# Kernel optimization log

Measured on AMD Instinct MI355X. Metric: run time of the kernel, lower is better.

## Reference

```python
import jax, jax.numpy as jnp
import numpy as np


def setup_inputs() -> dict:
    key = jax.random.key(0)
    ks = jax.random.split(key, 8)
    B, L, E, U = 32, 2048, 1024, 1024
    s = 0.02
    return {
        "dec_hidden": jax.random.normal(ks[0], (B, E), jnp.float32),
        "enc_output": jax.random.normal(ks[1], (B, L, E), jnp.float32),
        "prev_coverage": jax.random.uniform(ks[2], (B, L, 1), jnp.float32),
        "Ws_k": jax.random.normal(ks[3], (E, U), jnp.float32) * s,
        "Ws_b": jnp.zeros((U,), jnp.float32),
        "Wh_k": jax.random.normal(ks[4], (E, U), jnp.float32) * s,
        "Wh_b": jnp.zeros((U,), jnp.float32),
        "Wc_k": jax.random.normal(ks[5], (1, U), jnp.float32) * s,
        "Wc_b": jnp.zeros((U,), jnp.float32),
        "V_k": jax.random.normal(ks[6], (U, 1), jnp.float32) * s,
        "V_b": jnp.zeros((1,), jnp.float32),
        "enc_pad_mask": jnp.ones((B, L), jnp.int32),
        "use_coverage": 1,
    }


def reference(dec_hidden, enc_output, prev_coverage, Ws_k, Ws_b, Wh_k, Wh_b,
              Wc_k, Wc_b, V_k, V_b, enc_pad_mask, use_coverage):
    # projections: [B,L,U] + [B,1,U] (+ [B,L,U] coverage term)
    pre = jnp.einsum('ble,eu->blu', enc_output, Ws_k) + Ws_b \
        + (dec_hidden @ Wh_k + Wh_b)[:, None, :]
    if use_coverage:
        pre = pre + (prev_coverage @ Wc_k + Wc_b)
    score = jnp.tanh(pre) @ V_k + V_b              # [B, L, 1]
    mask = enc_pad_mask.astype(score.dtype)        # [B, L]
    masked_score = (score[..., 0] * mask)[..., None]  # [B, L, 1]
    attention_weights = jax.nn.softmax(masked_score, axis=1)
    coverage = attention_weights + prev_coverage if use_coverage else attention_weights
    context_vector = jnp.sum(attention_weights * enc_output, axis=1)  # [B, E]
    return (context_vector, attention_weights, coverage)
```

## Files before the change

### kernel.cpp

```cpp
#include <hip/hip_runtime.h>
#include <hip/hip_bf16.h>
#include <math.h>

typedef float f32x4 __attribute__((ext_vector_type(4)));
typedef short short8 __attribute__((ext_vector_type(8)));
typedef unsigned short u16x8 __attribute__((ext_vector_type(8)));

static __device__ __forceinline__ unsigned short f2bf(float f) {
    unsigned u = __builtin_bit_cast(unsigned, f);
    unsigned r = (u + 0x7FFFu + ((u >> 16) & 1u)) >> 16;
    return (unsigned short)r;
}
static __device__ __forceinline__ float bf2f(unsigned short h) {
    unsigned u = ((unsigned)h) << 16;
    return __builtin_bit_cast(float, u);
}
static __device__ __forceinline__ float fast_tanh(float x) {
    float ax = fminf(fmaxf(x, -9.f), 9.f);
    float e = __expf(2.f * ax);
    return 1.f - 2.f / (e + 1.f);
}

#define GLD16(g, l) __builtin_amdgcn_global_load_lds(                        \
    (const __attribute__((address_space(1))) void*)(g),                      \
    (__attribute__((address_space(3))) void*)(l), 16, 0, 0)

__global__ __launch_bounds__(256) void prep_kernel(
    const float* __restrict__ enc, unsigned short* __restrict__ encB,
    const float* __restrict__ ws, unsigned short* __restrict__ wst,
    const float* __restrict__ dh, const float* __restrict__ whk,
    float* __restrict__ base_part)
{
    __shared__ unsigned short tile[64][65];
    __shared__ float dS[128];
    const int bid = blockIdx.x, tid = threadIdx.x;

    if (bid < 16384) {
        const size_t base0 = (size_t)bid * 4096;
#pragma unroll
        for (int i = 0; i < 4; i++) {
            size_t g = base0 + (size_t)i * 1024 + tid * 4;
            f32x4 v = *(const f32x4*)(enc + g);
            ushort4 w;
            w.x = f2bf(v.x); w.y = f2bf(v.y); w.z = f2bf(v.z); w.w = f2bf(v.w);
            *(ushort4*)(encB + g) = w;
        }
    } else if (bid < 16640) {
        const int b2 = bid - 16384;
        const int e0 = (b2 & 15) * 64, u0 = (b2 >> 4) * 64;
#pragma unroll
        for (int i = 0; i < 16; i++) {
            int idx = i * 256 + tid;
            int r = idx >> 6, c = idx & 63;
            tile[r][c] = f2bf(ws[(size_t)(e0 + r) * 1024 + u0 + c]);
        }
        __syncthreads();
#pragma unroll
        for (int i = 0; i < 16; i++) {
            int idx = i * 256 + tid;
            int r = idx >> 6, c = idx & 63;
            wst[(size_t)(u0 + r) * 1024 + e0 + c] = tile[c][r];
        }
    } else {
        const int b3 = bid - 16640;
        const int b = b3 & 31, ec = b3 >> 5;
        const int e0 = ec * 128;
        if (tid < 128) dS[tid] = dh[b * 1024 + e0 + tid];
        __syncthreads();
        f32x4 acc = {0.f, 0.f, 0.f, 0.f};
#pragma unroll 4
        for (int e = 0; e < 128; e++)
            acc += dS[e] * *(const f32x4*)(whk + (size_t)(e0 + e) * 1024 + tid * 4);
        *(f32x4*)(base_part + (size_t)ec * 32768 + b * 1024 + tid * 4) = acc;
    }
}

#define BM 128
#define BN 128
#define BK 32

__global__ __launch_bounds__(256) void score_gemm_fast(
    const unsigned short* __restrict__ encB,
    const unsigned short* __restrict__ wst,
    const float* __restrict__ base_part,
    const float* __restrict__ cov,
    const float* __restrict__ wc,
    const float* __restrict__ vk,
    const float* __restrict__ wsb, const float* __restrict__ whb,
    const float* __restrict__ wcb,
    const int* __restrict__ ucov,
    float* __restrict__ score_part)
{
    __shared__ unsigned short As[BM * BK];
    __shared__ unsigned short Bs[BN * BK];
    __shared__ float covS[BM];
    __shared__ float sred[2][BM];

    const int tid  = threadIdx.x;
    const int row0 = blockIdx.x * BM;
    const int u0   = blockIdx.y * BN;
    const int b    = row0 >> 11;
    const int use_cov = *ucov;

    if (tid < BM) covS[tid] = use_cov ? cov[row0 + tid] : 0.f;

    const int lane = tid & 63;
    const int wid  = tid >> 6;
    const int wm   = wid >> 1, wn = wid & 1;
    const int l16  = lane & 15, quad = lane >> 4;

    const int f0 = tid, f1 = 256 + tid;
    const int rA0 = f0 >> 2, rA1 = f1 >> 2;
    const int cA0 = ((f0 & 3) - rA0 - (rA0 >> 2)) & 3;
    const int cA1 = ((f1 & 3) - rA1 - (rA1 >> 2)) & 3;
    const unsigned short* pA0 = encB + (size_t)(row0 + rA0) * 1024 + cA0 * 8;
    const unsigned short* pA1 = encB + (size_t)(row0 + rA1) * 1024 + cA1 * 8;
    const unsigned short* pB0 = wst + (size_t)(u0 + rA0) * 1024 + cA0 * 8;
    const unsigned short* pB1 = wst + (size_t)(u0 + rA1) * 1024 + cA1 * 8;
    unsigned short* dA0 = As + f0 * 8;
    unsigned short* dA1 = As + f1 * 8;
    unsigned short* dB0 = Bs + f0 * 8;
    unsigned short* dB1 = Bs + f1 * 8;

    int offA[4], offB[4];
#pragma unroll
    for (int t = 0; t < 4; t++) {
        int ra = wm * 64 + t * 16 + l16;
        offA[t] = (ra * 4 + ((quad + ra + (ra >> 2)) & 3)) * 8;
        int rb = wn * 64 + t * 16 + l16;
        offB[t] = (rb * 4 + ((quad + rb + (rb >> 2)) & 3)) * 8;
    }

    f32x4 acc[4][4] = {};

    for (int kk = 0; kk < 1024 / BK; kk++) {
        __syncthreads();
        GLD16(pA0, dA0);
        GLD16(pA1, dA1);
        GLD16(pB0, dB0);
        GLD16(pB1, dB1);
        pA0 += BK; pA1 += BK; pB0 += BK; pB1 += BK;
        __syncthreads();

        short8 a[4], bb[4];
#pragma unroll
        for (int t = 0; t < 4; t++) {
            a[t]  = *(const short8*)&As[offA[t]];
            bb[t] = *(const short8*)&Bs[offB[t]];
        }
#pragma unroll
        for (int i = 0; i < 4; i++)
#pragma unroll
            for (int j = 0; j < 4; j++)
                acc[i][j] = __builtin_amdgcn_mfma_f32_16x16x32_bf16(a[i], bb[j], acc[i][j], 0, 0, 0);
    }

    float basev[4], wcv[4], vv[4];
#pragma unroll
    for (int j = 0; j < 4; j++) {
        int u = u0 + wn * 64 + j * 16 + l16;
        float bsum = wsb[u] + whb[u] + (use_cov ? wcb[u] : 0.f);
#pragma unroll
        for (int p = 0; p < 8; p++) bsum += base_part[p * 32768 + b * 1024 + u];
        basev[j] = bsum;
        wcv[j]   = use_cov ? wc[u] : 0.f;
        vv[j]    = vk[u];
    }
#pragma unroll
    for (int i = 0; i < 4; i++) {
        float part[4] = {0.f, 0.f, 0.f, 0.f};
#pragma unroll
        for (int r = 0; r < 4; r++) {
            float cv = covS[wm * 64 + i * 16 + quad * 4 + r];
#pragma unroll
            for (int j = 0; j < 4; j++)
                part[r] += fast_tanh(acc[i][j][r] + basev[j] + cv * wcv[j]) * vv[j];
        }
#pragma unroll
        for (int r = 0; r < 4; r++) {
            float v = part[r];
            v += __shfl_xor(v, 1);
            v += __shfl_xor(v, 2);
            v += __shfl_xor(v, 4);
            v += __shfl_xor(v, 8);
            if (l16 == 0) sred[wn][wm * 64 + i * 16 + quad * 4 + r] = v;
        }
    }
    __syncthreads();
    if (tid < BM)
        score_part[(size_t)blockIdx.y * 65536 + row0 + tid] = sred[0][tid] + sred[1][tid];
}

#define LDT 40
__global__ __launch_bounds__(256) void score_gemm_f32(
    const float* __restrict__ enc, const unsigned short* __restrict__ wst,
    const float* __restrict__ base_part, const float* __restrict__ cov,
    const float* __restrict__ wc, const float* __restrict__ vk,
    const float* __restrict__ wsb, const float* __restrict__ whb,
    const float* __restrict__ wcb,
    const int* __restrict__ ucov, float* __restrict__ score)
{
    __shared__ unsigned short As[BM * LDT];
    __shared__ unsigned short Bs[BN * LDT];
    __shared__ float covS[BM];
    const int tid = threadIdx.x;
    const int row0 = blockIdx.x * BM, u0 = blockIdx.y * BN;
    const int b = row0 >> 11;
    const int use_cov = *ucov;
    if (tid < BM) covS[tid] = use_cov ? cov[row0 + tid] : 0.f;
    const int lane = tid & 63, wid = tid >> 6;
    const int wm = wid >> 1, wn = wid & 1;
    const int l16 = lane & 15, quad = lane >> 4;
    f32x4 acc[4][4] = {};
    for (int k0 = 0; k0 < 1024; k0 += BK) {
        __syncthreads();
#pragma unroll
        for (int i = 0; i < 4; i++) {
            int f = i * 256 + tid;
            int r = f >> 3, c4 = f & 7;
            const float* p = enc + (size_t)(row0 + r) * 1024 + k0 + c4 * 4;
            ushort4 w;
            w.x = f2bf(p[0]); w.y = f2bf(p[1]); w.z = f2bf(p[2]); w.w = f2bf(p[3]);
            *(ushort4*)&As[r * LDT + c4 * 4] = w;
        }
#pragma unroll
        for (int i = 0; i < 2; i++) {
            int f = i * 256 + tid;
            int r = f >> 2, c8 = f & 3;
            uint4 w = *(const uint4*)(wst + (size_t)(u0 + r) * 1024 + k0 + c8 * 8);
            *(uint4*)&Bs[r * LDT + c8 * 8] = w;
        }
        __syncthreads();
        short8 a[4], bb[4];
#pragma unroll
        for (int t = 0; t < 4; t++) {
            a[t]  = *(const short8*)&As[(wm * 64 + t * 16 + l16) * LDT + quad * 8];
            bb[t] = *(const short8*)&Bs[(wn * 64 + t * 16 + l16) * LDT + quad * 8];
        }
#pragma unroll
        for (int i = 0; i < 4; i++)
#pragma unroll
            for (int j = 0; j < 4; j++)
                acc[i][j] = __builtin_amdgcn_mfma_f32_16x16x32_bf16(a[i], bb[j], acc[i][j], 0, 0, 0);
    }
    float basev[4], wcv[4], vv[4];
#pragma unroll
    for (int j = 0; j < 4; j++) {
        int u = u0 + wn * 64 + j * 16 + l16;
        float bsum = wsb[u] + whb[u] + (use_cov ? wcb[u] : 0.f);
#pragma unroll
        for (int p = 0; p < 8; p++) bsum += base_part[p * 32768 + b * 1024 + u];
        basev[j] = bsum;
        wcv[j] = use_cov ? wc[u] : 0.f;
        vv[j] = vk[u];
    }
#pragma unroll
    for (int i = 0; i < 4; i++) {
        float part[4] = {0.f, 0.f, 0.f, 0.f};
#pragma unroll
        for (int r = 0; r < 4; r++) {
            float cv = covS[wm * 64 + i * 16 + quad * 4 + r];
#pragma unroll
            for (int j = 0; j < 4; j++)
                part[r] += fast_tanh(acc[i][j][r] + basev[j] + cv * wcv[j]) * vv[j];
        }
#pragma unroll
        for (int r = 0; r < 4; r++) {
            float v = part[r];
            v += __shfl_xor(v, 1);
            v += __shfl_xor(v, 2);
            v += __shfl_xor(v, 4);
            v += __shfl_xor(v, 8);
            if (l16 == 0)
                atomicAdd(&score[row0 + wm * 64 + i * 16 + quad * 4 + r], v);
        }
    }
}

__global__ __launch_bounds__(1024) void softmax_kernel(
    const float* __restrict__ score_part, int nplanes,
    const float* __restrict__ vb,
    const int* __restrict__ mask, const float* __restrict__ cov,
    const int* __restrict__ ucov,
    float* __restrict__ attn_out, float* __restrict__ cov_out)
{
    __shared__ float redA[16], redB[16];
    __shared__ float bc0, bc1;
    const int b = blockIdx.x, tid = threadIdx.x;
    const int i0 = b * 2048 + tid, i1 = i0 + 1024;
    const float vbv = vb[0];
    const int uc = *ucov;

    float s0 = 0.f, s1 = 0.f;
    for (int p = 0; p < nplanes; p++) {
        s0 += score_part[(size_t)p * 65536 + i0];
        s1 += score_part[(size_t)p * 65536 + i1];
    }
    s0 = (s0 + vbv) * (float)mask[i0];
    s1 = (s1 + vbv) * (float)mask[i1];

    float m = fmaxf(s0, s1);
#pragma unroll
    for (int off = 1; off < 64; off <<= 1) m = fmaxf(m, __shfl_xor(m, off));
    if ((tid & 63) == 0) redA[tid >> 6] = m;
    __syncthreads();
    if (tid < 16) {
        float v = redA[tid];
#pragma unroll
        for (int off = 1; off < 16; off <<= 1) v = fmaxf(v, __shfl_xor(v, off));
        if (tid == 0) bc0 = v;
    }
    __syncthreads();
    const float M = bc0;

    float e0 = __expf(s0 - M), e1 = __expf(s1 - M);
    float s = e0 + e1;
#pragma unroll
    for (int off = 1; off < 64; off <<= 1) s += __shfl_xor(s, off);
    if ((tid & 63) == 0) redB[tid >> 6] = s;
    __syncthreads();
    if (tid < 16) {
        float v = redB[tid];
#pragma unroll
        for (int off = 1; off < 16; off <<= 1) v += __shfl_xor(v, off);
        if (tid == 0) bc1 = v;
    }
    __syncthreads();
    const float inv = 1.f / bc1;

    float a0 = e0 * inv, a1 = e1 * inv;
    attn_out[i0] = a0;
    attn_out[i1] = a1;
    cov_out[i0] = a0 + (uc ? cov[i0] : 0.f);
    cov_out[i1] = a1 + (uc ? cov[i1] : 0.f);
}

__global__ __launch_bounds__(256) void context_bf16(const unsigned short* __restrict__ encB,
                                                    const float* __restrict__ attn,
                                                    float* __restrict__ ctx_part) {
    __shared__ float aS[128];
    __shared__ float cred[1024];
    const int b = blockIdx.x, lc = blockIdx.y, tid = threadIdx.x;
    const int l0 = lc * 128;
    if (tid < 128) aS[tid] = attn[b * 2048 + l0 + tid];
    __syncthreads();
    const int e8 = (tid & 127) * 8, r0 = tid >> 7;
    float acc[8] = {};
#pragma unroll 4
    for (int l = r0 * 64; l < r0 * 64 + 64; l++) {
        u16x8 w = *(const u16x8*)(encB + (size_t)(b * 2048 + l0 + l) * 1024 + e8);
        float a = aS[l];
#pragma unroll
        for (int j = 0; j < 8; j++) acc[j] = fmaf(a, bf2f(w[j]), acc[j]);
    }
    if (r0 == 1) {
#pragma unroll
        for (int j = 0; j < 8; j++) cred[e8 + j] = acc[j];
    }
    __syncthreads();
    if (r0 == 0) {
        float* o = ctx_part + (size_t)lc * 32768 + b * 1024 + e8;
#pragma unroll
        for (int j = 0; j < 8; j++) o[j] = acc[j] + cred[e8 + j];
    }
}

__global__ __launch_bounds__(1024) void ctx_reduce(const float* __restrict__ ctx_part,
                                                   float* __restrict__ out_ctx) {
    const int b = blockIdx.x, e = threadIdx.x;
    float s = 0.f;
#pragma unroll
    for (int p = 0; p < 16; p++) s += ctx_part[(size_t)p * 32768 + b * 1024 + e];
    out_ctx[b * 1024 + e] = s;
}

__global__ __launch_bounds__(256) void context_f32(const float* __restrict__ enc,
                                                   const float* __restrict__ attn,
                                                   float* __restrict__ ctx) {
    __shared__ float aS[128];
    const int b = blockIdx.x, lc = blockIdx.y, tid = threadIdx.x;
    const int l0 = lc * 128;
    if (tid < 128) aS[tid] = attn[b * 2048 + l0 + tid];
    __syncthreads();
    const float* p = enc + ((size_t)(b * 2048 + l0)) * 1024 + tid * 4;
    f32x4 acc = {0.f, 0.f, 0.f, 0.f};
#pragma unroll 4
    for (int l = 0; l < 128; l++) acc += *(const f32x4*)(p + (size_t)l * 1024) * aS[l];
    float* o = ctx + b * 1024 + tid * 4;
    atomicAdd(o + 0, acc.x);
    atomicAdd(o + 1, acc.y);
    atomicAdd(o + 2, acc.z);
    atomicAdd(o + 3, acc.w);
}

__global__ __launch_bounds__(256) void prep2_kernel(
    const float* __restrict__ ws, unsigned short* __restrict__ wst,
    const float* __restrict__ dh, const float* __restrict__ whk,
    float* __restrict__ base_part)
{
    __shared__ unsigned short tile[64][65];
    __shared__ float dS[128];
    const int bid = blockIdx.x, tid = threadIdx.x;
    if (bid < 256) {
        const int e0 = (bid & 15) * 64, u0 = (bid >> 4) * 64;
#pragma unroll
        for (int i = 0; i < 16; i++) {
            int idx = i * 256 + tid;
            int r = idx >> 6, c = idx & 63;
            tile[r][c] = f2bf(ws[(size_t)(e0 + r) * 1024 + u0 + c]);
        }
        __syncthreads();
#pragma unroll
        for (int i = 0; i < 16; i++) {
            int idx = i * 256 + tid;
            int r = idx >> 6, c = idx & 63;
            wst[(size_t)(u0 + r) * 1024 + e0 + c] = tile[c][r];
        }
    } else {
        const int b3 = bid - 256;
        const int b = b3 & 31, ec = b3 >> 5;
        const int e0 = ec * 128;
        if (tid < 128) dS[tid] = dh[b * 1024 + e0 + tid];
        __syncthreads();
        f32x4 acc = {0.f, 0.f, 0.f, 0.f};
#pragma unroll 4
        for (int e = 0; e < 128; e++)
            acc += dS[e] * *(const f32x4*)(whk + (size_t)(e0 + e) * 1024 + tid * 4);
        *(f32x4*)(base_part + (size_t)ec * 32768 + b * 1024 + tid * 4) = acc;
    }
}

extern "C" void kernel_launch(void* const* d_in, const int* in_sizes, int n_in,
                              void* d_out, int out_size, void* d_ws, size_t ws_size,
                              hipStream_t stream) {
    const float* dec_hidden = (const float*)d_in[0];
    const float* enc        = (const float*)d_in[1];
    const float* prev_cov   = (const float*)d_in[2];
    const float* Ws_k       = (const float*)d_in[3];
    const float* Ws_b       = (const float*)d_in[4];
    const float* Wh_k       = (const float*)d_in[5];
    const float* Wh_b       = (const float*)d_in[6];
    const float* Wc_k       = (const float*)d_in[7];
    const float* Wc_b       = (const float*)d_in[8];
    const float* V_k        = (const float*)d_in[9];
    const float* V_b        = (const float*)d_in[10];
    const int*   mask       = (const int*)d_in[11];
    const int*   ucov       = (const int*)d_in[12];

    float* out_ctx  = (float*)d_out;
    float* out_attn = out_ctx + 32 * 1024;
    float* out_cov  = out_attn + 65536;

    char* ws = (char*)d_ws;
    unsigned short* wst = (unsigned short*)ws;
    float* base_part  = (float*)(ws + 2097152);
    float* score_part = (float*)(ws + 3145728);
    float* ctx_part   = score_part;
    unsigned short* encB = (unsigned short*)(ws + 5242880);
    const size_t need_fast = 5242880 + (size_t)32 * 2048 * 1024 * 2;

    if (ws_size >= need_fast) {
        prep_kernel<<<16896, 256, 0, stream>>>(enc, encB, Ws_k, wst, dec_hidden, Wh_k, base_part);
        score_gemm_fast<<<dim3(512, 8), 256, 0, stream>>>(
            encB, wst, base_part, prev_cov, Wc_k, V_k, Ws_b, Wh_b, Wc_b, ucov, score_part);
        softmax_kernel<<<32, 1024, 0, stream>>>(score_part, 8, V_b, mask, prev_cov, ucov, out_attn, out_cov);
        context_bf16<<<dim3(32, 16), 256, 0, stream>>>(encB, out_attn, ctx_part);
        ctx_reduce<<<32, 1024, 0, stream>>>(ctx_part, out_ctx);
    } else {
        hipMemsetAsync(score_part, 0, 65536 * sizeof(float), stream);
        hipMemsetAsync(out_ctx, 0, 32 * 1024 * sizeof(float), stream);
        prep2_kernel<<<512, 256, 0, stream>>>(Ws_k, wst, dec_hidden, Wh_k, base_part);
        score_gemm_f32<<<dim3(512, 8), 256, 0, stream>>>(
            enc, wst, base_part, prev_cov, Wc_k, V_k, Ws_b, Wh_b, Wc_b, ucov, score_part);
        softmax_kernel<<<32, 1024, 0, stream>>>(score_part, 1, V_b, mask, prev_cov, ucov, out_attn, out_cov);
        context_f32<<<dim3(32, 16), 256, 0, stream>>>(enc, out_attn, out_ctx);
    }
}
```

Measured before the change: 668.8 us.

## Double-buffer score GEMM LDS tiles and fuse context reduction into one kernel

The fast score GEMM now double-buffers its LDS tiles: it issues the next k-slice's global-to-LDS loads before running the MFMAs on the current slice, so each step needs one barrier instead of two. Bias, coverage-weight and V vectors are precomputed once per block into shared memory rather than loaded per thread after the loop. The context kernel is reorganised so each block owns 64 embedding columns across all 2048 positions and writes the final output directly, which removes the partial-sum buffer and the separate ctx_reduce launch. The trade-off is double the LDS for the GEMM tiles and fewer, longer-running context blocks.

After: 651.5 us. 1.03x faster.

```diff
diff --git a/kernel.cpp b/kernel.cpp
--- a/kernel.cpp
+++ b/kernel.cpp
@@ -91,9 +91,10 @@
     const int* __restrict__ ucov,
     float* __restrict__ score_part)
 {
-    __shared__ unsigned short As[BM * BK];
-    __shared__ unsigned short Bs[BN * BK];
+    __shared__ unsigned short As[2][BM * BK];
+    __shared__ unsigned short Bs[2][BN * BK];
     __shared__ float covS[BM];
+    __shared__ float baseS[BN], wcS[BN], vvS[BN];
     __shared__ float sred[2][BM];
 
     const int tid  = threadIdx.x;
@@ -103,6 +104,15 @@
     const int use_cov = *ucov;
 
     if (tid < BM) covS[tid] = use_cov ? cov[row0 + tid] : 0.f;
+    if (tid < BN) {
+        int u = u0 + tid;
+        float s = wsb[u] + whb[u] + (use_cov ? wcb[u] : 0.f);
+#pragma unroll
+        for (int p = 0; p < 8; p++) s += base_part[p * 32768 + b * 1024 + u];
+        baseS[tid] = s;
+        wcS[tid]   = use_cov ? wc[u] : 0.f;
+        vvS[tid]   = vk[u];
+    }
 
     const int lane = tid & 63;
     const int wid  = tid >> 6;
@@ -117,10 +127,6 @@
     const unsigned short* pA1 = encB + (size_t)(row0 + rA1) * 1024 + cA1 * 8;
     const unsigned short* pB0 = wst + (size_t)(u0 + rA0) * 1024 + cA0 * 8;
     const unsigned short* pB1 = wst + (size_t)(u0 + rA1) * 1024 + cA1 * 8;
-    unsigned short* dA0 = As + f0 * 8;
-    unsigned short* dA1 = As + f1 * 8;
-    unsigned short* dB0 = Bs + f0 * 8;
-    unsigned short* dB1 = Bs + f1 * 8;
 
     int offA[4], offB[4];
 #pragma unroll
@@ -133,48 +139,49 @@
 
     f32x4 acc[4][4] = {};
 
-    for (int kk = 0; kk < 1024 / BK; kk++) {
-        __syncthreads();
-        GLD16(pA0, dA0);
-        GLD16(pA1, dA1);
-        GLD16(pB0, dB0);
-        GLD16(pB1, dB1);
-        pA0 += BK; pA1 += BK; pB0 += BK; pB1 += BK;
-        __syncthreads();
-
+    GLD16(pA0, &As[0][f0 * 8]);
+    GLD16(pA1, &As[0][f1 * 8]);
+    GLD16(pB0, &Bs[0][f0 * 8]);
+    GLD16(pB1, &Bs[0][f1 * 8]);
+    pA0 += BK; pA1 += BK; pB0 += BK; pB1 += BK;
+    __syncthreads();
+
+    for (int kk = 0; kk < 32; kk++) {
+        const int cur = kk & 1, nxt = cur ^ 1;
+        if (kk < 31) {
+            GLD16(pA0, &As[nxt][f0 * 8]);
+            GLD16(pA1, &As[nxt][f1 * 8]);
+            GLD16(pB0, &Bs[nxt][f0 * 8]);
+            GLD16(pB1, &Bs[nxt][f1 * 8]);
+            pA0 += BK; pA1 += BK; pB0 += BK; pB1 += BK;
+        }
         short8 a[4], bb[4];
 #pragma unroll
         for (int t = 0; t < 4; t++) {
-            a[t]  = *(const short8*)&As[offA[t]];
-            bb[t] = *(const short8*)&Bs[offB[t]];
+            a[t]  = *(const short8*)&As[cur][offA[t]];
+            bb[t] = *(const short8*)&Bs[cur][offB[t]];
         }
 #pragma unroll
         for (int i = 0; i < 4; i++)
 #pragma unroll
             for (int j = 0; j < 4; j++)
                 acc[i][j] = __builtin_amdgcn_mfma_f32_16x16x32_bf16(a[i], bb[j], acc[i][j], 0, 0, 0);
-    }
-
-    float basev[4], wcv[4], vv[4];
-#pragma unroll
-    for (int j = 0; j < 4; j++) {
-        int u = u0 + wn * 64 + j * 16 + l16;
-        float bsum = wsb[u] + whb[u] + (use_cov ? wcb[u] : 0.f);
-#pragma unroll
-        for (int p = 0; p < 8; p++) bsum += base_part[p * 32768 + b * 1024 + u];
-        basev[j] = bsum;
-        wcv[j]   = use_cov ? wc[u] : 0.f;
-        vv[j]    = vk[u];
-    }
+        __syncthreads();
+    }
+
 #pragma unroll
     for (int i = 0; i < 4; i++) {
         float part[4] = {0.f, 0.f, 0.f, 0.f};
 #pragma unroll
         for (int r = 0; r < 4; r++) {
-            float cv = covS[wm * 64 + i * 16 + quad * 4 + r];
-#pragma unroll
-            for (int j = 0; j < 4; j++)
-                part[r] += fast_tanh(acc[i][j][r] + basev[j] + cv * wcv[j]) * vv[j];
+            int rl = wm * 64 + i * 16 + quad * 4 + r;
+            float cv = covS[rl];
+#pragma unroll
+            for (int j = 0; j < 4; j++) {
+                int ul = wn * 64 + j * 16 + l16;
+                float pre = acc[i][j][r] + baseS[ul] + cv * wcS[ul];
+                part[r] += fast_tanh(pre) * vvS[ul];
+            }
         }
 #pragma unroll
         for (int r = 0; r < 4; r++) {
@@ -189,92 +196,6 @@
     __syncthreads();
     if (tid < BM)
         score_part[(size_t)blockIdx.y * 65536 + row0 + tid] = sred[0][tid] + sred[1][tid];
-}
-
-#define LDT 40
-__global__ __launch_bounds__(256) void score_gemm_f32(
-    const float* __restrict__ enc, const unsigned short* __restrict__ wst,
-    const float* __restrict__ base_part, const float* __restrict__ cov,
-    const float* __restrict__ wc, const float* __restrict__ vk,
-    const float* __restrict__ wsb, const float* __restrict__ whb,
-    const float* __restrict__ wcb,
-    const int* __restrict__ ucov, float* __restrict__ score)
-{
-    __shared__ unsigned short As[BM * LDT];
-    __shared__ unsigned short Bs[BN * LDT];
-    __shared__ float covS[BM];
-    const int tid = threadIdx.x;
-    const int row0 = blockIdx.x * BM, u0 = blockIdx.y * BN;
-    const int b = row0 >> 11;
-    const int use_cov = *ucov;
-    if (tid < BM) covS[tid] = use_cov ? cov[row0 + tid] : 0.f;
-    const int lane = tid & 63, wid = tid >> 6;
-    const int wm = wid >> 1, wn = wid & 1;
-    const int l16 = lane & 15, quad = lane >> 4;
-    f32x4 acc[4][4] = {};
-    for (int k0 = 0; k0 < 1024; k0 += BK) {
-        __syncthreads();
-#pragma unroll
-        for (int i = 0; i < 4; i++) {
-            int f = i * 256 + tid;
-            int r = f >> 3, c4 = f & 7;
-            const float* p = enc + (size_t)(row0 + r) * 1024 + k0 + c4 * 4;
-            ushort4 w;
-            w.x = f2bf(p[0]); w.y = f2bf(p[1]); w.z = f2bf(p[2]); w.w = f2bf(p[3]);
-            *(ushort4*)&As[r * LDT + c4 * 4] = w;
-        }
-#pragma unroll
-        for (int i = 0; i < 2; i++) {
-            int f = i * 256 + tid;
-            int r = f >> 2, c8 = f & 3;
-            uint4 w = *(const uint4*)(wst + (size_t)(u0 + r) * 1024 + k0 + c8 * 8);
-            *(uint4*)&Bs[r * LDT + c8 * 8] = w;
-        }
-        __syncthreads();
-        short8 a[4], bb[4];
-#pragma unroll
-        for (int t = 0; t < 4; t++) {
-            a[t]  = *(const short8*)&As[(wm * 64 + t * 16 + l16) * LDT + quad * 8];
-            bb[t] = *(const short8*)&Bs[(wn * 64 + t * 16 + l16) * LDT + quad * 8];
-        }
-#pragma unroll
-        for (int i = 0; i < 4; i++)
-#pragma unroll
-            for (int j = 0; j < 4; j++)
-                acc[i][j] = __builtin_amdgcn_mfma_f32_16x16x32_bf16(a[i], bb[j], acc[i][j], 0, 0, 0);
-    }
-    float basev[4], wcv[4], vv[4];
-#pragma unroll
-    for (int j = 0; j < 4; j++) {
-        int u = u0 + wn * 64 + j * 16 + l16;
-        float bsum = wsb[u] + whb[u] + (use_cov ? wcb[u] : 0.f);
-#pragma unroll
-        for (int p = 0; p < 8; p++) bsum += base_part[p * 32768 + b * 1024 + u];
-        basev[j] = bsum;
-        wcv[j] = use_cov ? wc[u] : 0.f;
-        vv[j] = vk[u];
-    }
-#pragma unroll
-    for (int i = 0; i < 4; i++) {
-        float part[4] = {0.f, 0.f, 0.f, 0.f};
-#pragma unroll
-        for (int r = 0; r < 4; r++) {
-            float cv = covS[wm * 64 + i * 16 + quad * 4 + r];
-#pragma unroll
-            for (int j = 0; j < 4; j++)
-                part[r] += fast_tanh(acc[i][j][r] + basev[j] + cv * wcv[j]) * vv[j];
-        }
-#pragma unroll
-        for (int r = 0; r < 4; r++) {
-            float v = part[r];
-            v += __shfl_xor(v, 1);
-            v += __shfl_xor(v, 2);
-            v += __shfl_xor(v, 4);
-            v += __shfl_xor(v, 8);
-            if (l16 == 0)
-                atomicAdd(&score[row0 + wm * 64 + i * 16 + quad * 4 + r], v);
-        }
-    }
 }
 
 __global__ __launch_bounds__(1024) void softmax_kernel(
@@ -337,41 +258,125 @@
 
 __global__ __launch_bounds__(256) void context_bf16(const unsigned short* __restrict__ encB,
                                                     const float* __restrict__ attn,
-                                                    float* __restrict__ ctx_part) {
-    __shared__ float aS[128];
-    __shared__ float cred[1024];
-    const int b = blockIdx.x, lc = blockIdx.y, tid = threadIdx.x;
-    const int l0 = lc * 128;
-    if (tid < 128) aS[tid] = attn[b * 2048 + l0 + tid];
-    __syncthreads();
-    const int e8 = (tid & 127) * 8, r0 = tid >> 7;
+                                                    float* __restrict__ out_ctx) {
+    __shared__ float aS[2048];
+    __shared__ float red[4][64];
+    const int b = blockIdx.x, ec = blockIdx.y, tid = threadIdx.x;
+    const int e0 = ec * 64;
+    for (int i = tid; i < 2048; i += 256) aS[i] = attn[b * 2048 + i];
+    __syncthreads();
+    const int es = (tid & 7) * 8;
+    const int lo = tid >> 3;
     float acc[8] = {};
-#pragma unroll 4
-    for (int l = r0 * 64; l < r0 * 64 + 64; l++) {
-        u16x8 w = *(const u16x8*)(encB + (size_t)(b * 2048 + l0 + l) * 1024 + e8);
+    for (int l = lo; l < 2048; l += 32) {
+        u16x8 w = *(const u16x8*)(encB + (size_t)(b * 2048 + l) * 1024 + e0 + es);
         float a = aS[l];
 #pragma unroll
         for (int j = 0; j < 8; j++) acc[j] = fmaf(a, bf2f(w[j]), acc[j]);
     }
-    if (r0 == 1) {
-#pragma unroll
-        for (int j = 0; j < 8; j++) cred[e8 + j] = acc[j];
-    }
-    __syncthreads();
-    if (r0 == 0) {
-        float* o = ctx_part + (size_t)lc * 32768 + b * 1024 + e8;
-#pragma unroll
-        for (int j = 0; j < 8; j++) o[j] = acc[j] + cred[e8 + j];
-    }
-}
-
-__global__ __launch_bounds__(1024) void ctx_reduce(const float* __restrict__ ctx_part,
-                                                   float* __restrict__ out_ctx) {
-    const int b = blockIdx.x, e = threadIdx.x;
-    float s = 0.f;
-#pragma unroll
-    for (int p = 0; p < 16; p++) s += ctx_part[(size_t)p * 32768 + b * 1024 + e];
-    out_ctx[b * 1024 + e] = s;
+#pragma unroll
+    for (int j = 0; j < 8; j++) {
+        float v = acc[j];
+        v += __shfl_xor(v, 8);
+        v += __shfl_xor(v, 16);
+        v += __shfl_xor(v, 32);
+        acc[j] = v;
+    }
+    const int wv = tid >> 6;
+    if ((tid & 63) < 8) {
+#pragma unroll
+        for (int j = 0; j < 8; j++) red[wv][(tid & 7) * 8 + j] = acc[j];
+    }
+    __syncthreads();
+    if (tid < 64)
+        out_ctx[b * 1024 + e0 + tid] = red[0][tid] + red[1][tid] + red[2][tid] + red[3][tid];
+}
+
+#define LDT 40
+__global__ __launch_bounds__(256) void score_gemm_f32(
+    const float* __restrict__ enc, const unsigned short* __restrict__ wst,
+    const float* __restrict__ base_part, const float* __restrict__ cov,
+    const float* __restrict__ wc, const float* __restrict__ vk,
+    const float* __restrict__ wsb, const float* __restrict__ whb,
+    const float* __restrict__ wcb,
+    const int* __restrict__ ucov, float* __restrict__ score)
+{
+    __shared__ unsigned short As[BM * LDT];
+    __shared__ unsigned short Bs[BN * LDT];
+    __shared__ float covS[BM];
+    __shared__ float baseS[BN], wcS[BN], vvS[BN];
+    const int tid = threadIdx.x;
+    const int row0 = blockIdx.x * BM, u0 = blockIdx.y * BN;
+    const int b = row0 >> 11;
+    const int use_cov = *ucov;
+    if (tid < BM) covS[tid] = use_cov ? cov[row0 + tid] : 0.f;
+    if (tid < BN) {
+        int u = u0 + tid;
+        float s = wsb[u] + whb[u] + (use_cov ? wcb[u] : 0.f);
+#pragma unroll
+        for (int p = 0; p < 8; p++) s += base_part[p * 32768 + b * 1024 + u];
+        baseS[tid] = s;
+        wcS[tid] = use_cov ? wc[u] : 0.f;
+        vvS[tid] = vk[u];
+    }
+    const int lane = tid & 63, wid = tid >> 6;
+    const int wm = wid >> 1, wn = wid & 1;
+    const int l16 = lane & 15, quad = lane >> 4;
+    f32x4 acc[4][4] = {};
+    for (int k0 = 0; k0 < 1024; k0 += BK) {
+        __syncthreads();
+#pragma unroll
+        for (int i = 0; i < 4; i++) {
+            int f = i * 256 + tid;
+            int r = f >> 3, c4 = f & 7;
+            const float* p = enc + (size_t)(row0 + r) * 1024 + k0 + c4 * 4;
+            ushort4 w;
+            w.x = f2bf(p[0]); w.y = f2bf(p[1]); w.z = f2bf(p[2]); w.w = f2bf(p[3]);
+            *(ushort4*)&As[r * LDT + c4 * 4] = w;
+        }
+#pragma unroll
+        for (int i = 0; i < 2; i++) {
+            int f = i * 256 + tid;
+            int r = f >> 2, c8 = f & 3;
+            uint4 w = *(const uint4*)(wst + (size_t)(u0 + r) * 1024 + k0 + c8 * 8);
+            *(uint4*)&Bs[r * LDT + c8 * 8] = w;
+        }
+        __syncthreads();
+        short8 a[4], bb[4];
+#pragma unroll
+        for (int t = 0; t < 4; t++) {
+            a[t]  = *(const short8*)&As[(wm * 64 + t * 16 + l16) * LDT + quad * 8];
+            bb[t] = *(const short8*)&Bs[(wn * 64 + t * 16 + l16) * LDT + quad * 8];
+        }
+#pragma unroll
+        for (int i = 0; i < 4; i++)
+#pragma unroll
+            for (int j = 0; j < 4; j++)
+                acc[i][j] = __builtin_amdgcn_mfma_f32_16x16x32_bf16(a[i], bb[j], acc[i][j], 0, 0, 0);
+    }
+#pragma unroll
+    for (int i = 0; i < 4; i++) {
+        float part[4] = {0.f, 0.f, 0.f, 0.f};
+#pragma unroll
+        for (int r = 0; r < 4; r++) {
+            float cv = covS[wm * 64 + i * 16 + quad * 4 + r];
+#pragma unroll
+            for (int j = 0; j < 4; j++) {
+                int ul = wn * 64 + j * 16 + l16;
+                part[r] += fast_tanh(acc[i][j][r] + baseS[ul] + cv * wcS[ul]) * vvS[ul];
+            }
+        }
+#pragma unroll
+        for (int r = 0; r < 4; r++) {
+            float v = part[r];
+            v += __shfl_xor(v, 1);
+            v += __shfl_xor(v, 2);
+            v += __shfl_xor(v, 4);
+            v += __shfl_xor(v, 8);
+            if (l16 == 0)
+                atomicAdd(&score[row0 + wm * 64 + i * 16 + quad * 4 + r], v);
+        }
+    }
 }
 
 __global__ __launch_bounds__(256) void context_f32(const float* __restrict__ enc,
@@ -455,7 +460,6 @@
     unsigned short* wst = (unsigned short*)ws;
     float* base_part  = (float*)(ws + 2097152);
     float* score_part = (float*)(ws + 3145728);
-    float* ctx_part   = score_part;
     unsigned short* encB = (unsigned short*)(ws + 5242880);
     const size_t need_fast = 5242880 + (size_t)32 * 2048 * 1024 * 2;
 
@@ -464,8 +468,7 @@
         score_gemm_fast<<<dim3(512, 8), 256, 0, stream>>>(
             encB, wst, base_part, prev_cov, Wc_k, V_k, Ws_b, Wh_b, Wc_b, ucov, score_part);
         softmax_kernel<<<32, 1024, 0, stream>>>(score_part, 8, V_b, mask, prev_cov, ucov, out_attn, out_cov);
-        context_bf16<<<dim3(32, 16), 256, 0, stream>>>(encB, out_attn, ctx_part);
-        ctx_reduce<<<32, 1024, 0, stream>>>(ctx_part, out_ctx);
+        context_bf16<<<dim3(32, 16), 256, 0, stream>>>(encB, out_attn, out_ctx);
     } else {
         hipMemsetAsync(score_part, 0, 65536 * sizeof(float), stream);
         hipMemsetAsync(out_ctx, 0, 32 * 1024 * sizeof(float), stream);
```
